# Performance work log

Measured on AMD Instinct MI355X. Metric: run time of the kernel, lower is better.

The kernel has to match this reference:

```python
import jax, jax.numpy as jnp
import numpy as np

N_HEADS = 8
TOPK = 32


def setup_inputs() -> dict:
    key = jax.random.key(0)
    ks = jax.random.split(key, 6)
    N, L, Hd = 2, 2048, 512
    s = 1.0 / np.sqrt(Hd).astype(np.float32)
    return {
        "queries": jax.random.normal(ks[0], (N, L, Hd), jnp.float32),
        "keys": jax.random.normal(ks[1], (N, L, Hd), jnp.float32),
        "values": jax.random.normal(ks[2], (N, L, Hd), jnp.float32),
        "Wq": jax.random.normal(ks[3], (Hd, Hd), jnp.float32) * s,
        "bq": jnp.zeros((Hd,), jnp.float32),
        "Wk": jax.random.normal(ks[4], (Hd, Hd), jnp.float32) * s,
        "bk": jnp.zeros((Hd,), jnp.float32),
        "Wv": jax.random.normal(ks[5], (Hd, Hd), jnp.float32) * s,
        "bv": jnp.zeros((Hd,), jnp.float32),
    }


def reference(queries, keys, values, Wq, bq, Wk, bk, Wv, bv):
    N, L, Hd = queries.shape
    S = keys.shape[1]
    H = N_HEADS
    E = Hd // H
    q = (queries @ Wq.T + bq).reshape(N, L, H, E)
    k = (keys @ Wk.T + bk).reshape(N, S, H, E)
    v = (values @ Wv.T + bv).reshape(N, S, H, E)
    temp = 1.0 / np.sqrt(E).astype(np.float32)
    QK = jnp.einsum("nlhe,nshe->nhls", q, k)  # [N,H,L,S]
    topk = min(TOPK, S)
    _, idx = jax.lax.top_k(QK, topk)  # idx: [N,H,L,topk]
    ni = jnp.arange(N)[:, None, None, None]
    hi = jnp.arange(H)[None, :, None, None]
    li = jnp.arange(L)[None, None, :, None]
    keep = jnp.zeros(QK.shape, bool).at[ni, hi, li, idx].set(True)
    # torch: softmax(temp * (QK + mask)) with mask 0 on top-k, -inf elsewhere
    scores = jnp.where(keep, temp * QK, -jnp.inf)
    A = jax.nn.softmax(scores, axis=-1)  # dropout is identity in eval mode
    V = jnp.einsum("nhls,nshd->nlhd", A, v).reshape(N, L, Hd)
    return V, A
```

## Files before the change

### kernel.cpp

```cpp
#include <hip/hip_runtime.h>
#include <cstdint>
#include <cstddef>
#include <math.h>

#define NH     8
#define EH     64
#define HD     512
#define NBATCH 2
#define LSEQ   2048
#define TK     32


using f32x4  = __attribute__((ext_vector_type(4))) float;
using bf16x8 = __attribute__((ext_vector_type(8))) short;
using u16x8  = __attribute__((ext_vector_type(8))) unsigned short;
using u16x4  = __attribute__((ext_vector_type(4))) unsigned short;

__device__ __forceinline__ unsigned short f2b(float f) {
    unsigned u = __float_as_uint(f);
    return (unsigned short)((u + 0x7FFFu + ((u >> 16) & 1u)) >> 16);
}
__device__ __forceinline__ unsigned f2key(float f) {
    unsigned u = __float_as_uint(f);
    return (u & 0x80000000u) ? ~u : (u | 0x80000000u);
}
__device__ __forceinline__ float key2f(unsigned k) {
    return __uint_as_float((k & 0x80000000u) ? (k ^ 0x80000000u) : ~k);
}
__device__ __forceinline__ unsigned umax2(unsigned a, unsigned b) { return a > b ? a : b; }
__device__ __forceinline__ int swzA(int r, int c) { return c ^ ((r >> 2) & 7); }
__device__ __forceinline__ int swzB(int r, int c) { return c ^ (((r >> 2) ^ (r >> 5)) & 7); }

__global__ __launch_bounds__(256, 3) void proj_kernel(
    const float* __restrict__ Xq, const float* __restrict__ Xk, const float* __restrict__ Xv,
    const float* __restrict__ Wq, const float* __restrict__ Bq,
    const float* __restrict__ Wk, const float* __restrict__ Bk,
    const float* __restrict__ Wv, const float* __restrict__ Bv,
    float* __restrict__ ws)
{
    const int z = blockIdx.z;
    const float* X = (z == 0) ? Xq : (z == 1) ? Xk : Xv;
    const float* W = (z == 0) ? Wq : (z == 1) ? Wk : Wv;
    const float* B = (z == 0) ? Bq : (z == 1) ? Bk : Bv;
    float* out = ws + (size_t)z * 2097152;
    unsigned short* khi = (unsigned short*)(ws + 6291456);

    __shared__ float4 Xs[64 * 8];
    __shared__ float4 Ws[128 * 8];
    __shared__ unsigned short kst[64 * 136];

    const int tid = threadIdx.x;
    const int tx = tid & 15, ty = tid >> 4;
    const int m0 = blockIdx.x * 64, n0 = blockIdx.y * 128;

    float acc[4][8];
    #pragma unroll
    for (int i = 0; i < 4; ++i)
        #pragma unroll
        for (int j = 0; j < 8; ++j) acc[i][j] = 0.f;

    for (int k0 = 0; k0 < HD; k0 += 32) {
        #pragma unroll
        for (int it = 0; it < 2; ++it) {
            int f = tid + it * 256;
            int row = f >> 3, c = f & 7;
            Xs[row * 8 + swzA(row, c)] = *(const float4*)&X[(size_t)(m0 + row) * HD + k0 + c * 4];
        }
        #pragma unroll
        for (int it = 0; it < 4; ++it) {
            int f = tid + it * 256;
            int row = f >> 3, c = f & 7;
            Ws[row * 8 + swzB(row, c)] = *(const float4*)&W[(size_t)(n0 + row) * HD + k0 + c * 4];
        }
        __syncthreads();
        #pragma unroll
        for (int c = 0; c < 8; ++c) {
            float4 av[4], bv[8];
            #pragma unroll
            for (int i = 0; i < 4; ++i) { int r = ty * 4 + i; av[i] = Xs[r * 8 + swzA(r, c)]; }
            #pragma unroll
            for (int j = 0; j < 8; ++j) { int r = tx * 8 + j; bv[j] = Ws[r * 8 + swzB(r, c)]; }
            #pragma unroll
            for (int i = 0; i < 4; ++i)
                #pragma unroll
                for (int j = 0; j < 8; ++j) {
                    acc[i][j] = fmaf(av[i].x, bv[j].x, acc[i][j]);
                    acc[i][j] = fmaf(av[i].y, bv[j].y, acc[i][j]);
                    acc[i][j] = fmaf(av[i].z, bv[j].z, acc[i][j]);
                    acc[i][j] = fmaf(av[i].w, bv[j].w, acc[i][j]);
                }
        }
        __syncthreads();
    }

    float4 bb[2];
    bb[0] = *(const float4*)&B[n0 + tx * 8 + 0];
    bb[1] = *(const float4*)&B[n0 + tx * 8 + 4];
    #pragma unroll
    for (int i = 0; i < 4; ++i) {
        int m = m0 + ty * 4 + i;
        int n = m >> 11, s = m & 2047;
        #pragma unroll
        for (int jj = 0; jj < 2; ++jj) {
            int o0 = n0 + tx * 8 + jj * 4;
            int head = n * NH + (o0 >> 6), e0 = o0 & 63;
            float4 val;
            val.x = acc[i][jj * 4 + 0] + bb[jj].x;
            val.y = acc[i][jj * 4 + 1] + bb[jj].y;
            val.z = acc[i][jj * 4 + 2] + bb[jj].z;
            val.w = acc[i][jj * 4 + 3] + bb[jj].w;
            *(float4*)&out[(size_t)head * 131072 + (size_t)s * EH + e0] = val;
            if (z == 1) {
                u16x4 b4;
                b4[0] = f2b(val.x); b4[1] = f2b(val.y);
                b4[2] = f2b(val.z); b4[3] = f2b(val.w);
                *(u16x4*)&kst[(ty * 4 + i) * 136 + tx * 8 + jj * 4] = b4;
            }
        }
    }

    if (z == 1) {
        __syncthreads();
        const int base_head = (m0 >> 11) * NH + (n0 >> 6);
        const int kt0 = (m0 & 2047) >> 4;
        #pragma unroll
        for (int it = 0; it < 4; ++it) {
            int g = tid + it * 256;
            int lane_g = g & 63;
            int rest = g >> 6;
            int head_loc = rest >> 3, ksb = (rest >> 2) & 1, kt = rest & 3;
            int s_loc = kt * 16 + (lane_g & 15);
            int ecol = head_loc * 64 + ksb * 32 + ((lane_g >> 4) << 3);
            u16x8 vv = *(const u16x8*)&kst[s_loc * 136 + ecol];
            size_t idx = ((((size_t)(base_head + head_loc) * 128 + (kt0 + kt)) * 2 + ksb) * 64 + lane_g) * 8;
            *(u16x8*)&khi[idx] = vv;
        }
    }
}

__device__ __forceinline__ unsigned long long sort64_desc(unsigned long long v, int lane) {
    #pragma unroll
    for (int k = 2; k <= 64; k <<= 1)
        #pragma unroll
        for (int j = k >> 1; j >= 1; j >>= 1) {
            unsigned long long o = __shfl_xor(v, j, 64);
            bool up = ((lane & k) != 0);
            bool keepmin = (((lane & j) == 0) == up);
            unsigned long long lo = v < o ? v : o;
            unsigned long long hi = v > o ? v : o;
            v = keepmin ? lo : hi;
        }
    return v;
}
__device__ __forceinline__ unsigned sort32_desc(unsigned v, int lane) {
    #pragma unroll
    for (int k = 2; k <= 64; k <<= 1)
        #pragma unroll
        for (int j = k >> 1; j >= 1; j >>= 1) {
            unsigned o = __shfl_xor(v, j, 64);
            bool up = ((lane & k) != 0);
            bool keepmin = (((lane & j) == 0) == up);
            unsigned lo = v < o ? v : o, hi = v > o ? v : o;
            v = keepmin ? lo : hi;
        }
    return v;
}
__device__ __forceinline__ unsigned long long merge_top64(unsigned long long a, unsigned long long b, int lane) {
    unsigned long long br = __shfl(b, 63 - lane, 64);
    unsigned long long m = a > br ? a : br;
    #pragma unroll
    for (int j = 32; j >= 1; j >>= 1) {
        unsigned long long o = __shfl_xor(m, j, 64);
        bool keepmax = ((lane & j) == 0);
        unsigned long long mx = m > o ? m : o;
        unsigned long long mn = m < o ? m : o;
        m = keepmax ? mx : mn;
    }
    return m;
}

__global__ __launch_bounds__(512, 4) void attn_kernel(
    const float* __restrict__ ws, float* __restrict__ outV, float* __restrict__ outA)
{
    const float* qw = ws;
    const float* kw = ws + 2097152;
    const float* vw = ws + 4194304;
    const unsigned short* khi = (const unsigned short*)(ws + 6291456);

    __shared__ unsigned short scores16[2048 * 16];
    __shared__ float qs[EH * 16];
    __shared__ unsigned short candArr[8 * 2 * 192];

    const int tid  = threadIdx.x;
    const int lane = tid & 63;
    const int uwv  = __builtin_amdgcn_readfirstlane(tid) >> 6;

    unsigned bid = blockIdx.x;
    unsigned id  = (bid & 7u) * 256u + (bid >> 3);
    const int head = (int)(id >> 7);
    const int l0   = (int)(id & 127u) * 16;
    const size_t headoff = (size_t)head * 131072;

    #pragma unroll
    for (int it = 0; it < 2; ++it) {
        int i = tid + it * 512;
        int row = i & 15, e = i >> 4;
        qs[i] = qw[headoff + (size_t)(l0 + row) * EH + e];
    }
    __syncthreads();

    {
        bf16x8 afrag[2];
        #pragma unroll
        for (int ks = 0; ks < 2; ++ks)
            #pragma unroll
            for (int j = 0; j < 8; ++j) {
                int e = ks * 32 + ((lane >> 4) << 3) + j;
                afrag[ks][j] = (short)f2b(qs[e * 16 + (lane & 15)]);
            }

        #pragma unroll
        for (int kt = 0; kt < 16; ++kt) {
            f32x4 acc = (f32x4)(0.f);
            int ktg = uwv * 16 + kt;
            #pragma unroll
            for (int ks = 0; ks < 2; ++ks) {
                bf16x8 b = *(const bf16x8*)(khi + (size_t)head * 131072 +
                              ((((size_t)ktg * 2 + ks) * 64 + lane) << 3));
                acc = __builtin_amdgcn_mfma_f32_16x16x32_bf16(afrag[ks], b, acc, 0, 0, 0);
            }
            int key = uwv * 256 + kt * 16 + (lane & 15);
            int rbase = (lane >> 4) << 2;
            int p = rbase ^ (key & 12);
            u16x4 s4;
            #pragma unroll
            for (int reg = 0; reg < 4; ++reg)
                s4[reg] = (unsigned short)(f2key(acc[reg]) >> 16);
            *(u16x4*)&scores16[key * 16 + p] = s4;
        }
    }
    __syncthreads();

    const unsigned long long lmlt = (1ull << lane) - 1ull;
    int selS[2]; float selW[2];

    const int r0 = 2 * uwv;
    unsigned pk[32];
    #pragma unroll
    for (int t = 0; t < 32; ++t) {
        int key = t * 64 + lane;
        int p0 = r0 ^ (key & 12);
        pk[t] = *(const unsigned*)&scores16[key * 16 + p0];
    }
    __syncthreads();

    #pragma unroll
    for (int rr2 = 0; rr2 < 2; ++rr2) {
        const int lrow = l0 + r0 + rr2;
        unsigned short* cand = candArr + (uwv * 2 + rr2) * 192;

        unsigned mx = 0;
        #pragma unroll
        for (int t = 0; t < 32; ++t) {
            unsigned a = rr2 ? (pk[t] >> 16) : (pk[t] & 0xFFFFu);
            mx = umax2(mx, a);
        }
        {
            unsigned v = mx;
            #pragma unroll
            for (int k = 2; k <= 64; k <<= 1)
                #pragma unroll
                for (int j = k >> 1; j >= 1; j >>= 1) {
                    unsigned o = __shfl_xor(v, j);
                    bool up = ((lane & k) == 0);
                    bool keepmin = (((lane & j) == 0) == up);
                    unsigned lo = v < o ? v : o, hi = v > o ? v : o;
                    v = keepmin ? lo : hi;
                }
            mx = __shfl(v, 32);
        }
        const unsigned tau16 = mx;
        const float tauf = key2f(tau16 << 16);
        const unsigned thr16 = f2key(tauf - 0.35f) >> 16;

        int Nc = 0;
        #pragma unroll
        for (int t = 0; t < 32; ++t) {
            unsigned a = rr2 ? (pk[t] >> 16) : (pk[t] & 0xFFFFu);
            bool c = a >= thr16;
            unsigned long long b = __ballot(c);
            if (c) {
                int p = Nc + __popcll(b & lmlt);
                if (p < 192) cand[p] = (unsigned short)(t * 64 + lane);
            }
            Nc += __popcll(b);
        }
        if (Nc > 192) Nc = 192;

        const float* qrow = qw + headoff + (size_t)lrow * EH;
        float4 qv[16];
        #pragma unroll
        for (int c4 = 0; c4 < 16; ++c4) qv[c4] = *(const float4*)&qrow[c4 * 4];

        if (Nc <= 64) {
            bool valid = lane < Nc;
            int si = valid ? (int)cand[lane] : 0;
            const float* krow = kw + headoff + (size_t)si * EH;
            float sc = 0.f;
            #pragma unroll
            for (int c4 = 0; c4 < 16; ++c4) {
                float4 kv = *(const float4*)&krow[c4 * 4];
                sc = fmaf(qv[c4].x, kv.x, sc);
                sc = fmaf(qv[c4].y, kv.y, sc);
                sc = fmaf(qv[c4].z, kv.z, sc);
                sc = fmaf(qv[c4].w, kv.w, sc);
            }
            unsigned k32 = valid ? f2key(sc) : 0u;
            unsigned sorted = sort32_desc(k32, lane);
            const unsigned T   = __builtin_amdgcn_readlane((int)sorted, 31);
            const unsigned M32 = __builtin_amdgcn_readlane((int)sorted, 0);
            unsigned long long bgt = __ballot(k32 > T);
            int needEq = TK - __popcll(bgt);
            unsigned long long beq = __ballot(valid && (k32 == T));
            int eqrank = __popcll(beq & lmlt);
            bool kept = valid && ((k32 > T) || ((k32 == T) && (eqrank < needEq)));
            const float M = key2f(M32);
            float ee = kept ? __expf(0.125f * (sc - M)) : 0.f;
            float Z = ee;
            #pragma unroll
            for (int d = 1; d < 64; d <<= 1) Z += __shfl_xor(Z, d);
            float w = ee / Z;
            unsigned long long bk = __ballot(kept);
            int rk = __popcll(bk & lmlt);
            int addr = kept ? (rk * 4) : 252;
            int psi = __builtin_amdgcn_ds_permute(addr, si);
            int pw  = __builtin_amdgcn_ds_permute(addr, __float_as_int(w));
            selS[rr2] = psi;
            selW[rr2] = __int_as_float(pw);
        } else {
            const int nch = (Nc + 63) >> 6;
            unsigned long long best = 0ull;
            for (int c = 0; c < nch; ++c) {
                int p = c * 64 + lane;
                bool valid = p < Nc;
                int si = valid ? (int)cand[p] : 0;
                const float* krow = kw + headoff + (size_t)si * EH;
                float sc = 0.f;
                #pragma unroll
                for (int c4 = 0; c4 < 16; ++c4) {
                    float4 kv = *(const float4*)&krow[c4 * 4];
                    sc = fmaf(qv[c4].x, kv.x, sc);
                    sc = fmaf(qv[c4].y, kv.y, sc);
                    sc = fmaf(qv[c4].z, kv.z, sc);
                    sc = fmaf(qv[c4].w, kv.w, sc);
                }
                unsigned long long comp = valid
                    ? ((((unsigned long long)f2key(sc)) << 32) | (unsigned)(~si))
                    : 0ull;
                comp = sort64_desc(comp, lane);
                best = (c == 0) ? comp : merge_top64(best, comp, lane);
            }
            unsigned key32 = (unsigned)(best >> 32);
            int si = (int)(~((unsigned)best)) & 2047;
            float sc = key2f(key32);
            float M = __shfl(sc, 0);
            float ee = (lane < TK) ? __expf(0.125f * (sc - M)) : 0.f;
            float Z = ee;
            #pragma unroll
            for (int d = 1; d < 64; d <<= 1) Z += __shfl_xor(Z, d);
            selS[rr2] = si;
            selW[rr2] = ee / Z;
        }
    }

    float* abuf = (float*)((char*)scores16 + uwv * 8192);
    {
        float4* ab4 = (float4*)abuf;
        const float4 z4 = make_float4(0.f, 0.f, 0.f, 0.f);
        #pragma unroll
        for (int u = 0; u < 8; ++u) ab4[u * 64 + lane] = z4;
    }
    #pragma unroll
    for (int rr2 = 0; rr2 < 2; ++rr2) {
        const int lrow = l0 + r0 + rr2;
        float4* ab4 = (float4*)abuf;
        if (lane < TK) abuf[selS[rr2]] = selW[rr2];
        float* Arow = outA + ((size_t)head * 2048 + lrow) * 2048;
        #pragma unroll
        for (int u = 0; u < 8; ++u)
            *(float4*)&Arow[(u * 64 + lane) * 4] = ab4[u * 64 + lane];
        if (lane < TK) abuf[selS[rr2]] = 0.f;

        float acc = 0.f;
        int   siv = selS[rr2];
        unsigned wbits = __float_as_uint(selW[rr2]);
        #pragma unroll
        for (int i = 0; i < TK; ++i) {
            int s_i   = __builtin_amdgcn_readlane(siv, i);
            float w_i = __uint_as_float((unsigned)__builtin_amdgcn_readlane((int)wbits, i));
            acc = fmaf(w_i, vw[headoff + (size_t)s_i * EH + lane], acc);
        }
        const int n = head >> 3, h = head & 7;
        outV[((size_t)(n * 2048 + lrow)) * 512 + h * 64 + lane] = acc;
    }
}

extern "C" void kernel_launch(void* const* d_in, const int* in_sizes, int n_in,
                              void* d_out, int out_size, void* d_ws, size_t ws_size,
                              hipStream_t stream)
{
    (void)in_sizes; (void)n_in; (void)out_size; (void)ws_size;
    const float* q  = (const float*)d_in[0];
    const float* k  = (const float*)d_in[1];
    const float* v  = (const float*)d_in[2];
    const float* Wq = (const float*)d_in[3];
    const float* bq = (const float*)d_in[4];
    const float* Wk = (const float*)d_in[5];
    const float* bk = (const float*)d_in[6];
    const float* Wv = (const float*)d_in[7];
    const float* bv = (const float*)d_in[8];
    float* ws   = (float*)d_ws;
    float* outV = (float*)d_out;
    float* outA = outV + (size_t)NBATCH * LSEQ * HD;

    proj_kernel<<<dim3(64, 4, 3), 256, 0, stream>>>(q, k, v, Wq, bq, Wk, bk, Wv, bv, ws);
    attn_kernel<<<dim3(2048, 1, 1), 512, 0, stream>>>(ws, outV, outA);
}
```

Baseline: 220.3 us.

## Use 16 waves per block with one query row per wave

```diff
diff --git a/kernel.cpp b/kernel.cpp
--- a/kernel.cpp
+++ b/kernel.cpp
@@ -179,7 +179,7 @@
     return m;
 }
 
-__global__ __launch_bounds__(512, 4) void attn_kernel(
+__global__ __launch_bounds__(1024, 8) void attn_kernel(
     const float* __restrict__ ws, float* __restrict__ outV, float* __restrict__ outA)
 {
     const float* qw = ws;
@@ -189,7 +189,7 @@
 
     __shared__ unsigned short scores16[2048 * 16];
     __shared__ float qs[EH * 16];
-    __shared__ unsigned short candArr[8 * 2 * 192];
+    __shared__ unsigned short candArr[16 * 192];
 
     const int tid  = threadIdx.x;
     const int lane = tid & 63;
@@ -201,11 +201,9 @@
     const int l0   = (int)(id & 127u) * 16;
     const size_t headoff = (size_t)head * 131072;
 
-    #pragma unroll
-    for (int it = 0; it < 2; ++it) {
-        int i = tid + it * 512;
-        int row = i & 15, e = i >> 4;
-        qs[i] = qw[headoff + (size_t)(l0 + row) * EH + e];
+    {
+        int row = tid & 15, e = tid >> 4;
+        qs[e * 16 + row] = qw[headoff + (size_t)(l0 + row) * EH + e];
     }
     __syncthreads();
 
@@ -220,16 +218,16 @@
             }
 
         #pragma unroll
-        for (int kt = 0; kt < 16; ++kt) {
+        for (int kt = 0; kt < 8; ++kt) {
             f32x4 acc = (f32x4)(0.f);
-            int ktg = uwv * 16 + kt;
+            int ktg = uwv * 8 + kt;
             #pragma unroll
             for (int ks = 0; ks < 2; ++ks) {
                 bf16x8 b = *(const bf16x8*)(khi + (size_t)head * 131072 +
                               ((((size_t)ktg * 2 + ks) * 64 + lane) << 3));
                 acc = __builtin_amdgcn_mfma_f32_16x16x32_bf16(afrag[ks], b, acc, 0, 0, 0);
             }
-            int key = uwv * 256 + kt * 16 + (lane & 15);
+            int key = ktg * 16 + (lane & 15);
             int rbase = (lane >> 4) << 2;
             int p = rbase ^ (key & 12);
             u16x4 s4;
@@ -242,27 +240,28 @@
     __syncthreads();
 
     const unsigned long long lmlt = (1ull << lane) - 1ull;
-    int selS[2]; float selW[2];
-
-    const int r0 = 2 * uwv;
+    const int r  = uwv;
+    const int pb = r & 14;
+    const int hi = r & 1;
+    int selS; float selW;
+
     unsigned pk[32];
     #pragma unroll
     for (int t = 0; t < 32; ++t) {
         int key = t * 64 + lane;
-        int p0 = r0 ^ (key & 12);
+        int p0 = pb ^ (key & 12);
         pk[t] = *(const unsigned*)&scores16[key * 16 + p0];
     }
     __syncthreads();
 
-    #pragma unroll
-    for (int rr2 = 0; rr2 < 2; ++rr2) {
-        const int lrow = l0 + r0 + rr2;
-        unsigned short* cand = candArr + (uwv * 2 + rr2) * 192;
+    {
+        const int lrow = l0 + r;
+        unsigned short* cand = candArr + uwv * 192;
 
         unsigned mx = 0;
         #pragma unroll
         for (int t = 0; t < 32; ++t) {
-            unsigned a = rr2 ? (pk[t] >> 16) : (pk[t] & 0xFFFFu);
+            unsigned a = hi ? (pk[t] >> 16) : (pk[t] & 0xFFFFu);
             mx = umax2(mx, a);
         }
         {
@@ -274,8 +273,8 @@
                     unsigned o = __shfl_xor(v, j);
                     bool up = ((lane & k) == 0);
                     bool keepmin = (((lane & j) == 0) == up);
-                    unsigned lo = v < o ? v : o, hi = v > o ? v : o;
-                    v = keepmin ? lo : hi;
+                    unsigned lo = v < o ? v : o, hi2 = v > o ? v : o;
+                    v = keepmin ? lo : hi2;
                 }
             mx = __shfl(v, 32);
         }
@@ -286,7 +285,7 @@
         int Nc = 0;
         #pragma unroll
         for (int t = 0; t < 32; ++t) {
-            unsigned a = rr2 ? (pk[t] >> 16) : (pk[t] & 0xFFFFu);
+            unsigned a = hi ? (pk[t] >> 16) : (pk[t] & 0xFFFFu);
             bool c = a >= thr16;
             unsigned long long b = __ballot(c);
             if (c) {
@@ -335,8 +334,8 @@
             int addr = kept ? (rk * 4) : 252;
             int psi = __builtin_amdgcn_ds_permute(addr, si);
             int pw  = __builtin_amdgcn_ds_permute(addr, __float_as_int(w));
-            selS[rr2] = psi;
-            selW[rr2] = __int_as_float(pw);
+            selS = psi;
+            selW = __int_as_float(pw);
         } else {
             const int nch = (Nc + 63) >> 6;
             unsigned long long best = 0ull;
@@ -368,32 +367,40 @@
             float Z = ee;
             #pragma unroll
             for (int d = 1; d < 64; d <<= 1) Z += __shfl_xor(Z, d);
-            selS[rr2] = si;
-            selW[rr2] = ee / Z;
-        }
-    }
-
-    float* abuf = (float*)((char*)scores16 + uwv * 8192);
-    {
+            selS = si;
+            selW = ee / Z;
+        }
+    }
+
+    float* abuf = (float*)((char*)scores16 + (uwv & 7) * 8192);
+    const int lrow = l0 + r;
+    float* Arow = outA + ((size_t)head * 2048 + lrow) * 2048;
+    const float4 z4 = make_float4(0.f, 0.f, 0.f, 0.f);
+
+    if (uwv < 8) {
         float4* ab4 = (float4*)abuf;
-        const float4 z4 = make_float4(0.f, 0.f, 0.f, 0.f);
         #pragma unroll
         for (int u = 0; u < 8; ++u) ab4[u * 64 + lane] = z4;
-    }
-    #pragma unroll
-    for (int rr2 = 0; rr2 < 2; ++rr2) {
-        const int lrow = l0 + r0 + rr2;
-        float4* ab4 = (float4*)abuf;
-        if (lane < TK) abuf[selS[rr2]] = selW[rr2];
-        float* Arow = outA + ((size_t)head * 2048 + lrow) * 2048;
+        if (lane < TK) abuf[selS] = selW;
         #pragma unroll
         for (int u = 0; u < 8; ++u)
             *(float4*)&Arow[(u * 64 + lane) * 4] = ab4[u * 64 + lane];
-        if (lane < TK) abuf[selS[rr2]] = 0.f;
-
+    }
+    __syncthreads();
+    if (uwv >= 8) {
+        float4* ab4 = (float4*)abuf;
+        #pragma unroll
+        for (int u = 0; u < 8; ++u) ab4[u * 64 + lane] = z4;
+        if (lane < TK) abuf[selS] = selW;
+        #pragma unroll
+        for (int u = 0; u < 8; ++u)
+            *(float4*)&Arow[(u * 64 + lane) * 4] = ab4[u * 64 + lane];
+    }
+
+    {
         float acc = 0.f;
-        int   siv = selS[rr2];
-        unsigned wbits = __float_as_uint(selW[rr2]);
+        int   siv = selS;
+        unsigned wbits = __float_as_uint(selW);
         #pragma unroll
         for (int i = 0; i < TK; ++i) {
             int s_i   = __builtin_amdgcn_readlane(siv, i);
@@ -424,5 +431,5 @@
     float* outA = outV + (size_t)NBATCH * LSEQ * HD;
 
     proj_kernel<<<dim3(64, 4, 3), 256, 0, stream>>>(q, k, v, Wq, bq, Wk, bk, Wv, bv, ws);
-    attn_kernel<<<dim3(2048, 1, 1), 512, 0, stream>>>(ws, outV, outA);
-}
+    attn_kernel<<<dim3(2048, 1, 1), 1024, 0, stream>>>(ws, outV, outA);
+}
```

Result: slower. 231.6 us (+5.2%).
